# Optimization experiments

Measured on AMD Instinct MI355X. Metric: run time of the kernel, lower is better.

The kernel has to match this reference:

```python
import jax, jax.numpy as jnp
import numpy as np

_EPSILON = 1e-06
EPS = 0.05
MAX_ITER = 50
THRESHOLD = 0.001


def setup_inputs() -> dict:
    key = jax.random.key(0)
    k1, k2 = jax.random.split(key)
    source = jax.random.normal(k1, (8192, 64), dtype=jnp.float32)
    target = jax.random.normal(k2, (8192, 64), dtype=jnp.float32)
    return {"source": source, "target": target}


def _sinkhorn(source, target):
    source = source.astype(jnp.float32)
    target = target.astype(jnp.float32)
    # squared euclidean cost matrix [N, M] (cdist(p=2)**2)
    sq_s = jnp.sum(source * source, axis=1, keepdims=True)          # [N,1]
    sq_t = jnp.sum(target * target, axis=1, keepdims=True).T        # [1,M]
    cost = sq_s + sq_t - 2.0 * (source @ target.T)                  # [N,M]
    cost = jnp.maximum(cost, 0.0)

    n_source, n_target = cost.shape
    log_mu = jnp.full((n_source,), jnp.log(jnp.maximum(1.0 / n_source, _EPSILON)), dtype=jnp.float32)
    log_nu = jnp.full((n_target,), jnp.log(jnp.maximum(1.0 / n_target, _EPSILON)), dtype=jnp.float32)

    u0 = jnp.zeros((n_source,), dtype=jnp.float32)
    v0 = jnp.zeros((n_target,), dtype=jnp.float32)

    def step(carry, _):
        u, v, done = carry
        prev_u = u
        mc = (-cost + u[:, None] + v[None, :]) / EPS
        u_new = EPS * (log_mu - jax.nn.logsumexp(mc, axis=1)) + u
        mc2 = (-cost + u_new[:, None] + v[None, :]) / EPS
        v_new = EPS * (log_nu - jax.nn.logsumexp(mc2, axis=0)) + v
        # freeze state once converged (emulates the torch early break)
        u = jnp.where(done, u, u_new)
        v = jnp.where(done, v, v_new)
        done = done | (jnp.mean(jnp.abs(u_new - prev_u)) < THRESHOLD)
        return (u, v, done), None

    (u, v, _), _ = jax.lax.scan(step, (u0, v0, jnp.array(False)), None, length=MAX_ITER)

    transport_plan = jnp.exp((-cost + u[:, None] + v[None, :]) / EPS)
    return jnp.sum(transport_plan * cost)


def reference(source, target):
    return _sinkhorn(source, target)
```

## Files before the change

kernel.cpp:

```cpp
#include <hip/hip_runtime.h>

#define N      8192
#define KDIM   64
#define SCALE2     28.853900817779268f
#define INV_SCALE2 0.034657359027997264f
#define TWOSCALE   57.707801635558536f
#define EPSLN2     0.034657359027997264f
#define EPS_LOG_MU (-0.45054566736396444f)
#define THRESH     0.001f
#define NEG_BIG    (-1e30f)
#define NCHUNK  32
#define COLSPAN 256
#define NCT     16
#define NBUF    5
#define ROWS_PER_BLOCK 256

typedef __attribute__((ext_vector_type(8))) short bf16x8;
typedef __attribute__((ext_vector_type(4))) float f32x4;

static __device__ __forceinline__ float exp2fast(float x) { return __builtin_amdgcn_exp2f(x); }
static __device__ __forceinline__ float log2fast(float x) { return __builtin_amdgcn_logf(x); }

static __device__ __forceinline__ unsigned short f2bf(float f) {
    unsigned u = __float_as_uint(f);
    u += 0x7FFFu + ((u >> 16) & 1u);
    return (unsigned short)(u >> 16);
}
static __device__ __forceinline__ float bf2f(unsigned short h) {
    return __uint_as_float(((unsigned)h) << 16);
}

static __device__ __forceinline__ void load16_to_lds(const void* gptr, void* lptr) {
    __builtin_amdgcn_global_load_lds(
        (const __attribute__((address_space(1))) unsigned int*)gptr,
        (__attribute__((address_space(3))) unsigned int*)lptr,
        16, 0, 0);
}

static __device__ __forceinline__ void stage_tile(
        const unsigned short* __restrict__ CPhi, const unsigned short* __restrict__ CPlo,
        char* ldsbuf, int jb, int wave, int swz) {
    const char* gsrc = (const char*)(wave < 2 ? CPhi : CPlo);
    const char* g = gsrc + (size_t)jb * 128 + (size_t)((wave & 1) * 1024 + swz);
    char* l = ldsbuf + (wave & 1) * 1024 + (wave >> 1) * 2048;
    load16_to_lds(g, l);
}

static __device__ __forceinline__ void load_held(
        const unsigned short* __restrict__ RPhi, const unsigned short* __restrict__ RPlo,
        int rowbase, int lrow, int kgrp, bf16x8 (&bh)[4][2], bf16x8 (&bl)[4][2]) {
#pragma unroll
    for (int it = 0; it < 4; ++it)
#pragma unroll
        for (int ks = 0; ks < 2; ++ks) {
            int boff = (rowbase + it * 16 + lrow) * KDIM + ks * 32 + kgrp * 8;
            bh[it][ks] = *reinterpret_cast<const bf16x8*>(RPhi + boff);
            bl[it][ks] = *reinterpret_cast<const bf16x8*>(RPlo + boff);
            asm volatile("" : "+v"(bh[it][ks]));
            asm volatile("" : "+v"(bl[it][ks]));
        }
}

static __device__ __forceinline__ void barrier_lds_only() {
    asm volatile("s_waitcnt lgkmcnt(0)" ::: "memory");
    __builtin_amdgcn_sched_barrier(0);
    __builtin_amdgcn_s_barrier();
    __builtin_amdgcn_sched_barrier(0);
}

static __device__ __forceinline__ void pipe_wait(int n) {
    if (n >= 3)      asm volatile("s_waitcnt vmcnt(3)" ::: "memory");
    else if (n == 2) asm volatile("s_waitcnt vmcnt(2)" ::: "memory");
    else if (n == 1) asm volatile("s_waitcnt vmcnt(1)" ::: "memory");
    else             asm volatile("s_waitcnt vmcnt(0)" ::: "memory");
    __builtin_amdgcn_sched_barrier(0);
    __builtin_amdgcn_s_barrier();
    __builtin_amdgcn_sched_barrier(0);
}

static __device__ __forceinline__ void lse_loop(
        const unsigned short* __restrict__ CPhi, const unsigned short* __restrict__ CPlo,
        char* ldsA, const float* lds_alpha,
        const bf16x8 (&bh)[4][2], const bf16x8 (&bl)[4][2],
        int jbase0, int wave, int lane, int swz, float (&m)[4], float (&s)[4]) {
    const int lrow = lane & 15, kgrp = lane >> 4;
    const int ro = lrow * 128;
    const int x0 = ((kgrp)     ^ (lrow & 7)) * 16;
    const int x1 = ((kgrp + 4) ^ (lrow & 7)) * 16;
#pragma unroll
    for (int ct = 0; ct < NCT; ++ct) {
        int w = NCT - 1 - ct; if (w > 3) w = 3;
        pipe_wait(w);
        if (ct + 4 < NCT)
            stage_tile(CPhi, CPlo, ldsA + ((ct + 4) % NBUF) * 4096,
                       jbase0 + (ct + 4) * 16, wave, swz);

        float4 av = *reinterpret_cast<const float4*>(lds_alpha + ct * 16 + kgrp * 4);
        const char* base = ldsA + (ct % NBUF) * 4096;
        bf16x8 ah0 = *reinterpret_cast<const bf16x8*>(base + ro + x0);
        bf16x8 ah1 = *reinterpret_cast<const bf16x8*>(base + ro + x1);
        bf16x8 al0 = *reinterpret_cast<const bf16x8*>(base + 2048 + ro + x0);
        bf16x8 al1 = *reinterpret_cast<const bf16x8*>(base + 2048 + ro + x1);

        __builtin_amdgcn_s_setprio(1);
        f32x4 acc[4];
#pragma unroll
        for (int it = 0; it < 4; ++it) {
            f32x4 a = {0.0f, 0.0f, 0.0f, 0.0f};
            a = __builtin_amdgcn_mfma_f32_16x16x32_bf16(ah0, bh[it][0], a, 0, 0, 0);
            a = __builtin_amdgcn_mfma_f32_16x16x32_bf16(ah1, bh[it][1], a, 0, 0, 0);
            a = __builtin_amdgcn_mfma_f32_16x16x32_bf16(al0, bh[it][0], a, 0, 0, 0);
            a = __builtin_amdgcn_mfma_f32_16x16x32_bf16(al1, bh[it][1], a, 0, 0, 0);
            a = __builtin_amdgcn_mfma_f32_16x16x32_bf16(ah0, bl[it][0], a, 0, 0, 0);
            a = __builtin_amdgcn_mfma_f32_16x16x32_bf16(ah1, bl[it][1], a, 0, 0, 0);
            acc[it] = a;
        }
        __builtin_amdgcn_s_setprio(0);

#pragma unroll
        for (int it = 0; it < 4; ++it) {
            float L0 = fmaf(TWOSCALE, acc[it][0], av.x);
            float L1 = fmaf(TWOSCALE, acc[it][1], av.y);
            float L2 = fmaf(TWOSCALE, acc[it][2], av.z);
            float L3 = fmaf(TWOSCALE, acc[it][3], av.w);
            float mx = fmaxf(fmaxf(L0, L1), fmaxf(L2, L3));
            float mn = fmaxf(m[it], mx);
            float rs = exp2fast(m[it] - mn);
            float e  = (exp2fast(L0 - mn) + exp2fast(L1 - mn)) +
                       (exp2fast(L2 - mn) + exp2fast(L3 - mn));
            s[it] = fmaf(s[it], rs, e);
            m[it] = mn;
        }
    }
}

static __device__ __forceinline__ void write_partials(
        float (&m)[4], float (&s)[4], float* __restrict__ pm, float* __restrict__ ps,
        const float* __restrict__ sqr2, int ck, int rowbase, int lane) {
    const int lrow = lane & 15, kgrp = lane >> 4;
#pragma unroll
    for (int off = 16; off < 64; off <<= 1) {
#pragma unroll
        for (int it = 0; it < 4; ++it) {
            float mo = __shfl_xor(m[it], off);
            float so = __shfl_xor(s[it], off);
            float mn = fmaxf(m[it], mo);
            s[it] = s[it] * exp2fast(m[it] - mn) + so * exp2fast(mo - mn);
            m[it] = mn;
        }
    }
    if (kgrp == 0) {
#pragma unroll
        for (int it = 0; it < 4; ++it) {
            int row = rowbase + it * 16 + lrow;
            pm[(size_t)ck * N + row] = m[it] - sqr2[row];
            ps[(size_t)ck * N + row] = s[it];
        }
    }
}

static __device__ __forceinline__ bool conv_done(const float* __restrict__ bd) {
    float sd = 0.0f;
#pragma unroll
    for (int c = 0; c < 32; ++c) sd += bd[c];
    return sd * (1.0f / (float)N) < THRESH;
}

__global__ void norms_kernel(const float* __restrict__ S, const float* __restrict__ T,
                             float* __restrict__ sq_s2, float* __restrict__ sq_t2) {
    int t = blockIdx.x * blockDim.x + threadIdx.x;
    const float* p = (t < N) ? S : T;
    int r = t & (N - 1);
    const float4* row = reinterpret_cast<const float4*>(p + (size_t)r * KDIM);
    float acc = 0.0f;
#pragma unroll
    for (int q = 0; q < KDIM / 4; ++q) {
        float4 a = row[q];
        acc += a.x * a.x + a.y * a.y + a.z * a.z + a.w * a.w;
    }
    if (t < N) sq_s2[r] = acc * SCALE2; else sq_t2[r] = acc * SCALE2;
}

__global__ void init_kernel(float* u, float* v, float* blockDiff) {
    int t = blockIdx.x * blockDim.x + threadIdx.x;
    if (t < N) { u[t] = 0.0f; v[t] = 0.0f; }
    if (t < 128) blockDiff[t] = 1.0e9f;
}

__global__ void split_kernel(const float* __restrict__ S, const float* __restrict__ T,
                             unsigned short* __restrict__ Shi, unsigned short* __restrict__ Slo,
                             unsigned short* __restrict__ Thi, unsigned short* __restrict__ Tlo) {
    int t = blockIdx.x * 256 + threadIdx.x;
    const int half = (N * KDIM) / 4;
    const float* src = (t < half) ? S : T;
    unsigned short* dhi = (t < half) ? Shi : Thi;
    unsigned short* dlo = (t < half) ? Slo : Tlo;
    int e = (t < half) ? t : t - half;
    float4 x = reinterpret_cast<const float4*>(src)[e];
    unsigned short h0 = f2bf(x.x), h1 = f2bf(x.y), h2 = f2bf(x.z), h3 = f2bf(x.w);
    ushort4 hv = make_ushort4(h0, h1, h2, h3);
    ushort4 lv = make_ushort4(f2bf(x.x - bf2f(h0)), f2bf(x.y - bf2f(h1)),
                              f2bf(x.z - bf2f(h2)), f2bf(x.w - bf2f(h3)));
    reinterpret_cast<ushort4*>(dhi)[e] = hv;
    reinterpret_cast<ushort4*>(dlo)[e] = lv;
}

__global__ __launch_bounds__(256, 4) void row_lse(
        const unsigned short* __restrict__ CPhi, const unsigned short* __restrict__ CPlo,
        const unsigned short* __restrict__ RPhi, const unsigned short* __restrict__ RPlo,
        const float* __restrict__ pmV, const float* __restrict__ psV,
        const float* __restrict__ sqc2,
        const float* __restrict__ sqr2,
        float* __restrict__ pm, float* __restrict__ ps,
        const float* __restrict__ bdPrev, int first) {
    if (!first && conv_done(bdPrev)) return;
    __shared__ __align__(16) char ldsA[NBUF * 4096];
    __shared__ __align__(16) float lds_alpha[COLSPAN];
    const int wave = threadIdx.x >> 6, lane = threadIdx.x & 63;
    const int lrow = lane & 15, kgrp = lane >> 4;
    const int ck = blockIdx.x & 31, rb = blockIdx.x >> 5;
    const int rowbase = rb * ROWS_PER_BLOCK + wave * 64;
    const int jbase0 = ck * COLSPAN;
    const int swz = (lane >> 3) * 128 + (((lane & 7) ^ ((lane >> 3) & 7)) << 4);

#pragma unroll
    for (int t = 0; t < 4; ++t)
        stage_tile(CPhi, CPlo, ldsA + t * 4096, jbase0 + t * 16, wave, swz);

    {
        int j = jbase0 + threadIdx.x;
        float a;
        if (first) {
            a = -sqc2[j];
        } else {
            float mm = NEG_BIG, ss = 0.0f;
#pragma unroll
            for (int c = 0; c < NCHUNK; ++c) {
                float mc = pmV[(size_t)c * N + j];
                float sc = psV[(size_t)c * N + j];
                float mn = fmaxf(mm, mc);
                ss = ss * exp2fast(mm - mn) + sc * exp2fast(mc - mn);
                mm = mn;
            }
            float vnew = EPS_LOG_MU - EPSLN2 * (mm + log2fast(ss));
            a = fmaf(vnew, SCALE2, -sqc2[j]);
        }
        lds_alpha[threadIdx.x] = a;
    }

    bf16x8 bh[4][2], bl[4][2];
    load_held(RPhi, RPlo, rowbase, lrow, kgrp, bh, bl);

    float m[4] = {NEG_BIG, NEG_BIG, NEG_BIG, NEG_BIG};
    float s[4] = {0.0f, 0.0f, 0.0f, 0.0f};
    barrier_lds_only();

    lse_loop(CPhi, CPlo, ldsA, lds_alpha, bh, bl, jbase0, wave, lane, swz, m, s);
    write_partials(m, s, pm, ps, sqr2, ck, rowbase, lane);
}

__global__ __launch_bounds__(256, 4) void col_lse(
        const unsigned short* __restrict__ CPhi, const unsigned short* __restrict__ CPlo,
        const unsigned short* __restrict__ RPhi, const unsigned short* __restrict__ RPlo,
        const float* __restrict__ pm_in, const float* __restrict__ ps_in,
        const float* __restrict__ sqs2,
        float* __restrict__ u,
        const float* __restrict__ bdPrev,
        float* __restrict__ bdCur,
        const float* __restrict__ sqr2,
        float* __restrict__ pm, float* __restrict__ ps) {
    const int ck = blockIdx.x & 31, rb = blockIdx.x >> 5;
    if (conv_done(bdPrev)) {
        if (rb == 0 && threadIdx.x == 0) bdCur[ck] = 0.0f;
        return;
    }
    __shared__ __align__(16) char ldsA[NBUF * 4096];
    __shared__ __align__(16) float lds_alpha[COLSPAN];
    __shared__ float wsum[4];
    const int wave = threadIdx.x >> 6, lane = threadIdx.x & 63;
    const int lrow = lane & 15, kgrp = lane >> 4;
    const int rowbase = rb * ROWS_PER_BLOCK + wave * 64;
    const int jbase0 = ck * COLSPAN;
    const int swz = (lane >> 3) * 128 + (((lane & 7) ^ ((lane >> 3) & 7)) << 4);

#pragma unroll
    for (int t = 0; t < 4; ++t)
        stage_tile(CPhi, CPlo, ldsA + t * 4096, jbase0 + t * 16, wave, swz);

    {
        int j = jbase0 + threadIdx.x;
        float mm = NEG_BIG, ss = 0.0f;
#pragma unroll
        for (int c = 0; c < NCHUNK; ++c) {
            float mc = pm_in[(size_t)c * N + j];
            float sc = ps_in[(size_t)c * N + j];
            float mn = fmaxf(mm, mc);
            ss = ss * exp2fast(mm - mn) + sc * exp2fast(mc - mn);
            mm = mn;
        }
        float unew = EPS_LOG_MU - EPSLN2 * (mm + log2fast(ss));
        lds_alpha[threadIdx.x] = fmaf(unew, SCALE2, -sqs2[j]);
        if (rb == 0) {
            float d = fabsf(unew - u[j]);
            u[j] = unew;
#pragma unroll
            for (int off = 32; off; off >>= 1) d += __shfl_xor(d, off);
            if (lane == 0) wsum[wave] = d;
        }
    }

    bf16x8 bh[4][2], bl[4][2];
    load_held(RPhi, RPlo, rowbase, lrow, kgrp, bh, bl);

    float m[4] = {NEG_BIG, NEG_BIG, NEG_BIG, NEG_BIG};
    float s[4] = {0.0f, 0.0f, 0.0f, 0.0f};
    barrier_lds_only();
    if (rb == 0 && threadIdx.x == 0)
        bdCur[ck] = wsum[0] + wsum[1] + wsum[2] + wsum[3];

    lse_loop(CPhi, CPlo, ldsA, lds_alpha, bh, bl, jbase0, wave, lane, swz, m, s);
    write_partials(m, s, pm, ps, sqr2, ck, rowbase, lane);
}

__global__ __launch_bounds__(256) void v_final(const float* __restrict__ pm,
                                               const float* __restrict__ ps,
                                               float* __restrict__ v) {
    int j = blockIdx.x * 256 + threadIdx.x;
    float m = NEG_BIG, s = 0.0f;
#pragma unroll
    for (int c = 0; c < NCHUNK; ++c) {
        float mc = pm[(size_t)c * N + j];
        float sc = ps[(size_t)c * N + j];
        float mn = fmaxf(m, mc);
        s = s * exp2fast(m - mn) + sc * exp2fast(mc - mn);
        m = mn;
    }
    v[j] = EPS_LOG_MU - EPSLN2 * (m + log2fast(s));
}

__global__ __launch_bounds__(256, 4) void plan_mfma(
        const unsigned short* __restrict__ CPhi, const unsigned short* __restrict__ CPlo,
        const unsigned short* __restrict__ RPhi, const unsigned short* __restrict__ RPlo,
        const float* __restrict__ u, const float* __restrict__ v,
        const float* __restrict__ sqr2, const float* __restrict__ sqc2,
        float* __restrict__ part) {
    __shared__ __align__(16) char ldsA[NBUF * 4096];
    __shared__ __align__(16) float lds_v2[COLSPAN];
    __shared__ __align__(16) float lds_sqc[COLSPAN];
    __shared__ float wsum[4];
    const int wave = threadIdx.x >> 6, lane = threadIdx.x & 63;
    const int lrow = lane & 15, kgrp = lane >> 4;
    const int ck = blockIdx.x & 31, rb = blockIdx.x >> 5;
    const int rowbase = rb * ROWS_PER_BLOCK + wave * 64;
    const int jbase0 = ck * COLSPAN;
    const int swz = (lane >> 3) * 128 + (((lane & 7) ^ ((lane >> 3) & 7)) << 4);

#pragma unroll
    for (int t = 0; t < 4; ++t)
        stage_tile(CPhi, CPlo, ldsA + t * 4096, jbase0 + t * 16, wave, swz);
    lds_v2[threadIdx.x]  = v[jbase0 + threadIdx.x] * SCALE2;
    lds_sqc[threadIdx.x] = sqc2[jbase0 + threadIdx.x];

    bf16x8 bh[4][2], bl[4][2];
    load_held(RPhi, RPlo, rowbase, lrow, kgrp, bh, bl);

    float sqr_i[4], u2_i[4];
#pragma unroll
    for (int it = 0; it < 4; ++it) {
        int row = rowbase + it * 16 + lrow;
        sqr_i[it] = sqr2[row];
        u2_i[it]  = u[row] * SCALE2;
    }

    float lsum = 0.0f;
    barrier_lds_only();

    const int ro = lrow * 128;
    const int x0 = ((kgrp)     ^ (lrow & 7)) * 16;
    const int x1 = ((kgrp + 4) ^ (lrow & 7)) * 16;
#pragma unroll
    for (int ct = 0; ct < NCT; ++ct) {
        int w = NCT - 1 - ct; if (w > 3) w = 3;
        pipe_wait(w);
        if (ct + 4 < NCT)
            stage_tile(CPhi, CPlo, ldsA + ((ct + 4) % NBUF) * 4096,
                       jbase0 + (ct + 4) * 16, wave, swz);

        float4 v2 = *reinterpret_cast<const float4*>(lds_v2 + ct * 16 + kgrp * 4);
        float4 sc = *reinterpret_cast<const float4*>(lds_sqc + ct * 16 + kgrp * 4);
        const char* base = ldsA + (ct % NBUF) * 4096;
        bf16x8 ah0 = *reinterpret_cast<const bf16x8*>(base + ro + x0);
        bf16x8 ah1 = *reinterpret_cast<const bf16x8*>(base + ro + x1);
        bf16x8 al0 = *reinterpret_cast<const bf16x8*>(base + 2048 + ro + x0);
        bf16x8 al1 = *reinterpret_cast<const bf16x8*>(base + 2048 + ro + x1);

        __builtin_amdgcn_s_setprio(1);
        f32x4 acc[4];
#pragma unroll
        for (int it = 0; it < 4; ++it) {
            f32x4 a = {0.0f, 0.0f, 0.0f, 0.0f};
            a = __builtin_amdgcn_mfma_f32_16x16x32_bf16(ah0, bh[it][0], a, 0, 0, 0);
            a = __builtin_amdgcn_mfma_f32_16x16x32_bf16(ah1, bh[it][1], a, 0, 0, 0);
            a = __builtin_amdgcn_mfma_f32_16x16x32_bf16(al0, bh[it][0], a, 0, 0, 0);
            a = __builtin_amdgcn_mfma_f32_16x16x32_bf16(al1, bh[it][1], a, 0, 0, 0);
            a = __builtin_amdgcn_mfma_f32_16x16x32_bf16(ah0, bl[it][0], a, 0, 0, 0);
            a = __builtin_amdgcn_mfma_f32_16x16x32_bf16(ah1, bl[it][1], a, 0, 0, 0);
            acc[it] = a;
        }
        __builtin_amdgcn_s_setprio(0);

        float vs[4] = {v2.x, v2.y, v2.z, v2.w};
        float ss[4] = {sc.x, sc.y, sc.z, sc.w};
#pragma unroll
        for (int it = 0; it < 4; ++it) {
#pragma unroll
            for (int r = 0; r < 4; ++r) {
                float c2 = fmaxf(sqr_i[it] + ss[r] - TWOSCALE * acc[it][r], 0.0f);
                lsum = fmaf(exp2fast(u2_i[it] + vs[r] - c2), c2, lsum);
            }
        }
    }
    lsum *= INV_SCALE2;

#pragma unroll
    for (int off = 32; off; off >>= 1) lsum += __shfl_xor(lsum, off);
    if (lane == 0) wsum[wave] = lsum;
    __syncthreads();
    if (threadIdx.x == 0)
        part[blockIdx.x] = wsum[0] + wsum[1] + wsum[2] + wsum[3];
}

__global__ void final_reduce(const float* __restrict__ part, float* __restrict__ out) {
    int t = threadIdx.x;
    float sum = 0.0f;
    for (int i = t; i < 1024; i += 256) sum += part[i];
#pragma unroll
    for (int off = 32; off; off >>= 1) sum += __shfl_xor(sum, off);
    __shared__ float wsum[4];
    int lane = t & 63, wave = t >> 6;
    if (lane == 0) wsum[wave] = sum;
    __syncthreads();
    if (t == 0) out[0] = wsum[0] + wsum[1] + wsum[2] + wsum[3];
}

extern "C" void kernel_launch(void* const* d_in, const int* in_sizes, int n_in,
                              void* d_out, int out_size, void* d_ws, size_t ws_size,
                              hipStream_t stream) {
    const float* S = (const float*)d_in[0];
    const float* T = (const float*)d_in[1];
    float* out = (float*)d_out;

    unsigned short* us = (unsigned short*)d_ws;
    unsigned short* Shi = us;
    unsigned short* Slo = us + (size_t)N * KDIM;
    unsigned short* Thi = us + (size_t)2 * N * KDIM;
    unsigned short* Tlo = us + (size_t)3 * N * KDIM;
    float* w = (float*)(us + (size_t)4 * N * KDIM);
    size_t off = 0;
    float* sq_s2     = w + off; off += N;
    float* sq_t2     = w + off; off += N;
    float* u         = w + off; off += N;
    float* v         = w + off; off += N;
    float* pmA       = w + off; off += (size_t)NCHUNK * N;
    float* psA       = w + off; off += (size_t)NCHUNK * N;
    float* pmB       = w + off; off += (size_t)NCHUNK * N;
    float* psB       = w + off; off += (size_t)NCHUNK * N;
    float* blockDiff = w + off; off += 128;
    float* part      = w + off; off += 1024;

    hipLaunchKernelGGL(norms_kernel, dim3(64),   dim3(256), 0, stream, S, T, sq_s2, sq_t2);
    hipLaunchKernelGGL(init_kernel,  dim3(32),   dim3(256), 0, stream, u, v, blockDiff);
    hipLaunchKernelGGL(split_kernel, dim3(1024), dim3(256), 0, stream, S, T, Shi, Slo, Thi, Tlo);

    const int LSE_BLOCKS = (N / ROWS_PER_BLOCK) * NCHUNK;
    for (int it = 0; it < 50; ++it) {
        float* bdPrev = blockDiff + ((it + 1) & 1) * 64;
        float* bdCur  = blockDiff + (it & 1) * 64;
        hipLaunchKernelGGL(row_lse, dim3(LSE_BLOCKS), dim3(256), 0, stream,
                           Thi, Tlo, Shi, Slo, pmB, psB, sq_t2, sq_s2,
                           pmA, psA, bdPrev, it == 0 ? 1 : 0);
        hipLaunchKernelGGL(col_lse, dim3(LSE_BLOCKS), dim3(256), 0, stream,
                           Shi, Slo, Thi, Tlo, pmA, psA, sq_s2, u,
                           bdPrev, bdCur, sq_t2, pmB, psB);
    }

    hipLaunchKernelGGL(v_final, dim3(32), dim3(256), 0, stream, pmB, psB, v);
    hipLaunchKernelGGL(plan_mfma, dim3(LSE_BLOCKS), dim3(256), 0, stream,
                       Thi, Tlo, Shi, Slo, u, v, sq_s2, sq_t2, part);
    hipLaunchKernelGGL(final_reduce, dim3(1), dim3(256), 0, stream, part, out);
}
```

Baseline: 3.277 ms.

## Give each wave a private double-buffered LDS tile stream, removing per-tile block barriers

Replaces the block-shared 5-deep tile ring, filled cooperatively by four waves and guarded by an s_barrier every column tile, with a private 2-buffer ring per wave. Each wave loads all four 1KB pieces of its own tiles and waits only on its own vmcnt, so no cross-wave barrier is needed inside the loop. The cost is four times the global-to-LDS traffic per block, since every wave fetches the same column tiles, plus a larger LDS footprint (32KB). Prefetch depth also drops from four tiles to two, which may expose more load latency.

New measurement: 3.402 ms. 3.8% more time.

```diff
diff --git a/kernel.cpp b/kernel.cpp
--- a/kernel.cpp
+++ b/kernel.cpp
@@ -12,7 +12,6 @@
 #define NCHUNK  32
 #define COLSPAN 256
 #define NCT     16
-#define NBUF    5
 #define ROWS_PER_BLOCK 256
 
 typedef __attribute__((ext_vector_type(8))) short bf16x8;
@@ -37,13 +36,15 @@
         16, 0, 0);
 }
 
-static __device__ __forceinline__ void stage_tile(
+static __device__ __forceinline__ void stage_tile_wave(
         const unsigned short* __restrict__ CPhi, const unsigned short* __restrict__ CPlo,
-        char* ldsbuf, int jb, int wave, int swz) {
-    const char* gsrc = (const char*)(wave < 2 ? CPhi : CPlo);
-    const char* g = gsrc + (size_t)jb * 128 + (size_t)((wave & 1) * 1024 + swz);
-    char* l = ldsbuf + (wave & 1) * 1024 + (wave >> 1) * 2048;
-    load16_to_lds(g, l);
+        char* buf, int jb, int swz) {
+    const char* gh = (const char*)CPhi + (size_t)jb * 128 + swz;
+    const char* gl = (const char*)CPlo + (size_t)jb * 128 + swz;
+    load16_to_lds(gh,        buf);
+    load16_to_lds(gh + 1024, buf + 1024);
+    load16_to_lds(gl,        buf + 2048);
+    load16_to_lds(gl + 1024, buf + 3072);
 }
 
 static __device__ __forceinline__ void load_held(
@@ -68,39 +69,31 @@
     __builtin_amdgcn_sched_barrier(0);
 }
 
-static __device__ __forceinline__ void pipe_wait(int n) {
-    if (n >= 3)      asm volatile("s_waitcnt vmcnt(3)" ::: "memory");
-    else if (n == 2) asm volatile("s_waitcnt vmcnt(2)" ::: "memory");
-    else if (n == 1) asm volatile("s_waitcnt vmcnt(1)" ::: "memory");
-    else             asm volatile("s_waitcnt vmcnt(0)" ::: "memory");
-    __builtin_amdgcn_sched_barrier(0);
-    __builtin_amdgcn_s_barrier();
-    __builtin_amdgcn_sched_barrier(0);
-}
-
 static __device__ __forceinline__ void lse_loop(
         const unsigned short* __restrict__ CPhi, const unsigned short* __restrict__ CPlo,
-        char* ldsA, const float* lds_alpha,
+        char* myLds, const float* lds_alpha,
         const bf16x8 (&bh)[4][2], const bf16x8 (&bl)[4][2],
-        int jbase0, int wave, int lane, int swz, float (&m)[4], float (&s)[4]) {
+        int jbase0, int lane, int swz, float (&m)[4], float (&s)[4]) {
     const int lrow = lane & 15, kgrp = lane >> 4;
     const int ro = lrow * 128;
     const int x0 = ((kgrp)     ^ (lrow & 7)) * 16;
     const int x1 = ((kgrp + 4) ^ (lrow & 7)) * 16;
 #pragma unroll
     for (int ct = 0; ct < NCT; ++ct) {
-        int w = NCT - 1 - ct; if (w > 3) w = 3;
-        pipe_wait(w);
-        if (ct + 4 < NCT)
-            stage_tile(CPhi, CPlo, ldsA + ((ct + 4) % NBUF) * 4096,
-                       jbase0 + (ct + 4) * 16, wave, swz);
-
+        if (ct < NCT - 1) asm volatile("s_waitcnt vmcnt(4)" ::: "memory");
+        else              asm volatile("s_waitcnt vmcnt(0)" ::: "memory");
+
+        const char* base = myLds + (ct & 1) * 4096;
         float4 av = *reinterpret_cast<const float4*>(lds_alpha + ct * 16 + kgrp * 4);
-        const char* base = ldsA + (ct % NBUF) * 4096;
         bf16x8 ah0 = *reinterpret_cast<const bf16x8*>(base + ro + x0);
         bf16x8 ah1 = *reinterpret_cast<const bf16x8*>(base + ro + x1);
         bf16x8 al0 = *reinterpret_cast<const bf16x8*>(base + 2048 + ro + x0);
         bf16x8 al1 = *reinterpret_cast<const bf16x8*>(base + 2048 + ro + x1);
+        asm volatile("s_waitcnt lgkmcnt(0)" ::: "memory");
+        asm volatile("" : "+v"(ah0), "+v"(ah1), "+v"(al0), "+v"(al1));
+        if (ct + 2 < NCT)
+            stage_tile_wave(CPhi, CPlo, myLds + (ct & 1) * 4096,
+                            jbase0 + (ct + 2) * 16, swz);
 
         __builtin_amdgcn_s_setprio(1);
         f32x4 acc[4];
@@ -214,7 +207,7 @@
         float* __restrict__ pm, float* __restrict__ ps,
         const float* __restrict__ bdPrev, int first) {
     if (!first && conv_done(bdPrev)) return;
-    __shared__ __align__(16) char ldsA[NBUF * 4096];
+    __shared__ __align__(16) char ldsA[4 * 8192];
     __shared__ __align__(16) float lds_alpha[COLSPAN];
     const int wave = threadIdx.x >> 6, lane = threadIdx.x & 63;
     const int lrow = lane & 15, kgrp = lane >> 4;
@@ -222,10 +215,10 @@
     const int rowbase = rb * ROWS_PER_BLOCK + wave * 64;
     const int jbase0 = ck * COLSPAN;
     const int swz = (lane >> 3) * 128 + (((lane & 7) ^ ((lane >> 3) & 7)) << 4);
-
-#pragma unroll
-    for (int t = 0; t < 4; ++t)
-        stage_tile(CPhi, CPlo, ldsA + t * 4096, jbase0 + t * 16, wave, swz);
+    char* myLds = ldsA + wave * 8192;
+
+    stage_tile_wave(CPhi, CPlo, myLds,        jbase0,      swz);
+    stage_tile_wave(CPhi, CPlo, myLds + 4096, jbase0 + 16, swz);
 
     {
         int j = jbase0 + threadIdx.x;
@@ -255,7 +248,7 @@
     float s[4] = {0.0f, 0.0f, 0.0f, 0.0f};
     barrier_lds_only();
 
-    lse_loop(CPhi, CPlo, ldsA, lds_alpha, bh, bl, jbase0, wave, lane, swz, m, s);
+    lse_loop(CPhi, CPlo, myLds, lds_alpha, bh, bl, jbase0, lane, swz, m, s);
     write_partials(m, s, pm, ps, sqr2, ck, rowbase, lane);
 }
 
@@ -274,7 +267,7 @@
         if (rb == 0 && threadIdx.x == 0) bdCur[ck] = 0.0f;
         return;
     }
-    __shared__ __align__(16) char ldsA[NBUF * 4096];
+    __shared__ __align__(16) char ldsA[4 * 8192];
     __shared__ __align__(16) float lds_alpha[COLSPAN];
     __shared__ float wsum[4];
     const int wave = threadIdx.x >> 6, lane = threadIdx.x & 63;
@@ -282,10 +275,10 @@
     const int rowbase = rb * ROWS_PER_BLOCK + wave * 64;
     const int jbase0 = ck * COLSPAN;
     const int swz = (lane >> 3) * 128 + (((lane & 7) ^ ((lane >> 3) & 7)) << 4);
-
-#pragma unroll
-    for (int t = 0; t < 4; ++t)
-        stage_tile(CPhi, CPlo, ldsA + t * 4096, jbase0 + t * 16, wave, swz);
+    char* myLds = ldsA + wave * 8192;
+
+    stage_tile_wave(CPhi, CPlo, myLds,        jbase0,      swz);
+    stage_tile_wave(CPhi, CPlo, myLds + 4096, jbase0 + 16, swz);
 
     {
         int j = jbase0 + threadIdx.x;
@@ -318,7 +311,7 @@
     if (rb == 0 && threadIdx.x == 0)
         bdCur[ck] = wsum[0] + wsum[1] + wsum[2] + wsum[3];
 
-    lse_loop(CPhi, CPlo, ldsA, lds_alpha, bh, bl, jbase0, wave, lane, swz, m, s);
+    lse_loop(CPhi, CPlo, myLds, lds_alpha, bh, bl, jbase0, lane, swz, m, s);
     write_partials(m, s, pm, ps, sqr2, ck, rowbase, lane);
 }
 
@@ -344,7 +337,7 @@
         const float* __restrict__ u, const float* __restrict__ v,
         const float* __restrict__ sqr2, const float* __restrict__ sqc2,
         float* __restrict__ part) {
-    __shared__ __align__(16) char ldsA[NBUF * 4096];
+    __shared__ __align__(16) char ldsA[4 * 8192];
     __shared__ __align__(16) float lds_v2[COLSPAN];
     __shared__ __align__(16) float lds_sqc[COLSPAN];
     __shared__ float wsum[4];
@@ -354,10 +347,10 @@
     const int rowbase = rb * ROWS_PER_BLOCK + wave * 64;
     const int jbase0 = ck * COLSPAN;
     const int swz = (lane >> 3) * 128 + (((lane & 7) ^ ((lane >> 3) & 7)) << 4);
-
-#pragma unroll
-    for (int t = 0; t < 4; ++t)
-        stage_tile(CPhi, CPlo, ldsA + t * 4096, jbase0 + t * 16, wave, swz);
+    char* myLds = ldsA + wave * 8192;
+
+    stage_tile_wave(CPhi, CPlo, myLds,        jbase0,      swz);
+    stage_tile_wave(CPhi, CPlo, myLds + 4096, jbase0 + 16, swz);
     lds_v2[threadIdx.x]  = v[jbase0 + threadIdx.x] * SCALE2;
     lds_sqc[threadIdx.x] = sqc2[jbase0 + threadIdx.x];
 
@@ -380,19 +373,21 @@
     const int x1 = ((kgrp + 4) ^ (lrow & 7)) * 16;
 #pragma unroll
     for (int ct = 0; ct < NCT; ++ct) {
-        int w = NCT - 1 - ct; if (w > 3) w = 3;
-        pipe_wait(w);
-        if (ct + 4 < NCT)
-            stage_tile(CPhi, CPlo, ldsA + ((ct + 4) % NBUF) * 4096,
-                       jbase0 + (ct + 4) * 16, wave, swz);
-
+        if (ct < NCT - 1) asm volatile("s_waitcnt vmcnt(4)" ::: "memory");
+        else              asm volatile("s_waitcnt vmcnt(0)" ::: "memory");
+
+        const char* base = myLds + (ct & 1) * 4096;
         float4 v2 = *reinterpret_cast<const float4*>(lds_v2 + ct * 16 + kgrp * 4);
         float4 sc = *reinterpret_cast<const float4*>(lds_sqc + ct * 16 + kgrp * 4);
-        const char* base = ldsA + (ct % NBUF) * 4096;
         bf16x8 ah0 = *reinterpret_cast<const bf16x8*>(base + ro + x0);
         bf16x8 ah1 = *reinterpret_cast<const bf16x8*>(base + ro + x1);
         bf16x8 al0 = *reinterpret_cast<const bf16x8*>(base + 2048 + ro + x0);
         bf16x8 al1 = *reinterpret_cast<const bf16x8*>(base + 2048 + ro + x1);
+        asm volatile("s_waitcnt lgkmcnt(0)" ::: "memory");
+        asm volatile("" : "+v"(ah0), "+v"(ah1), "+v"(al0), "+v"(al1));
+        if (ct + 2 < NCT)
+            stage_tile_wave(CPhi, CPlo, myLds + (ct & 1) * 4096,
+                            jbase0 + (ct + 2) * 16, swz);
 
         __builtin_amdgcn_s_setprio(1);
         f32x4 acc[4];
```
